# Kernel tuning notes

Measured on AMD Instinct MI355X. Metric: run time of the kernel, lower is better.

The kernel has to match this reference:

```python
import jax, jax.numpy as jnp
import numpy as np

N = 50000      # nodes
E = 1_600_000  # edges
F_IN = 128     # in_dim
H = 4          # heads
C = 32         # hidden_dim per head  (H*C == 128)
G = 64         # graphs in batch
HID2 = 64      # 2*hidden_dim
OUT = 10       # output_dim


def seg_softmax(logits, seg, num):
    # softmax over entries sharing the same segment id (leading axis)
    m = jax.ops.segment_max(logits, seg, num_segments=num)
    e = jnp.exp(logits - m[seg])
    s = jax.ops.segment_sum(e, seg, num_segments=num)
    return e / s[seg]


def gat_conv(x, src, dst, W, a_src, a_dst, b):
    # PyG GATConv (concat=True, negative_slope=0.2, self-loops added)
    h = (x @ W).reshape(N, H, C)                     # [N,H,C]
    loop = jnp.arange(N, dtype=src.dtype)
    s = jnp.concatenate([src, loop])                 # [E+N]
    d = jnp.concatenate([dst, loop])
    al_s = jnp.sum(h * a_src[None], axis=-1)         # [N,H]
    al_d = jnp.sum(h * a_dst[None], axis=-1)
    logits = jax.nn.leaky_relu(al_s[s] + al_d[d], 0.2)   # [E+N,H]
    alpha = seg_softmax(logits, d, N)                # softmax over incoming edges per dst
    msg = alpha[:, :, None] * h[s]                   # [E+N,H,C]
    out = jax.ops.segment_sum(msg, d, num_segments=N)    # [N,H,C]
    return out.reshape(N, H * C) + b


def setup_inputs() -> dict:
    key = jax.random.key(0)
    ks = jax.random.split(key, 16)
    x = jax.random.normal(ks[0], (N, F_IN), dtype=jnp.float32)
    src = jax.random.randint(ks[1], (E,), 0, N, dtype=jnp.int64)
    dst = jax.random.randint(ks[2], (E,), 0, N, dtype=jnp.int64)
    dst = jnp.where(src == dst, (dst + 1) % N, dst)  # GATConv removes self-loops then re-adds them
    edge_index = jnp.stack([src, dst])
    batch = jnp.sort(jax.random.randint(ks[3], (N,), 0, G, dtype=jnp.int64))
    g = lambda k, shp, fan: jax.random.normal(k, shp, dtype=jnp.float32) / np.sqrt(fan)
    return {
        "x": x, "edge_index": edge_index, "batch": batch,
        "W1": g(ks[4], (F_IN, H * C), F_IN), "a_src1": g(ks[5], (H, C), C), "a_dst1": g(ks[6], (H, C), C), "b1": jnp.zeros((H * C,), jnp.float32),
        "W2": g(ks[7], (H * C, H * C), H * C), "a_src2": g(ks[8], (H, C), C), "a_dst2": g(ks[9], (H, C), C), "b2": jnp.zeros((H * C,), jnp.float32),
        "gate_w": g(ks[10], (H * C, 1), H * C), "gate_b": jnp.zeros((1,), jnp.float32),
        "lin_w": g(ks[11], (H * C, HID2), H * C), "lin_b": jnp.zeros((HID2,), jnp.float32),
        "cls_w": g(ks[12], (HID2, OUT), HID2), "cls_b": jnp.zeros((OUT,), jnp.float32),
    }


def reference(x, edge_index, batch, W1, a_src1, a_dst1, b1, W2, a_src2, a_dst2, b2,
              gate_w, gate_b, lin_w, lin_b, cls_w, cls_b):
    src, dst = edge_index[0], edge_index[1]
    layers = [(W1, a_src1, a_dst1, b1), (W2, a_src2, a_dst2, b2)]
    hg = None
    h = x
    for (W, a_s, a_d, b) in layers:
        h = gat_conv(h, src, dst, W, a_s, a_d, b)
        h = jax.nn.relu(h)
        # per-graph softmax over nodes (dim=0 within each graph), per feature column
        h = seg_softmax(h, batch, G)
        # GlobalAttention pooling: gated segment-softmax sum
        gate = h @ gate_w + gate_b                    # [N,1]
        gate = seg_softmax(gate, batch, G)
        pooled = jax.ops.segment_sum(gate * h, batch, num_segments=G)  # [G, H*C]
        hg = pooled if hg is None else hg + pooled
    out = jax.nn.relu(hg @ lin_w + lin_b)             # dropout is identity in eval mode
    out = out @ cls_w + cls_b                         # [G, OUT]
    return out
```

## Files before the change

### kernel.cpp

```cpp
#include <hip/hip_runtime.h>
#include <hip/hip_fp16.h>
#include <math.h>

constexpr int N    = 50000;
constexpr int E    = 1600000;
constexpr int FD   = 128;
constexpr int H    = 4;
constexpr int G    = 64;
constexpr int NCH  = 16;
constexpr int OUT  = 10;

constexpr int NBIN   = (N + 255) / 256;
constexpr int EPB    = 4096;
constexpr int NBLK_E = (E + EPB - 1) / EPB;

#define DEV __device__ __forceinline__

DEV void fma4(float4& a, float s, const float4& w) {
    a.x = fmaf(s, w.x, a.x); a.y = fmaf(s, w.y, a.y);
    a.z = fmaf(s, w.z, a.z); a.w = fmaf(s, w.w, a.w);
}

DEV float lrelu_exp(float z) {
    return __expf(z > 0.f ? z : 0.2f * z);
}

union HF4 {
    float2  f;
    __half2 h[2];
};

DEV void fmah(float4& a, float w, const HF4& u) {
    float2 lo = __half22float2(u.h[0]);
    float2 hi = __half22float2(u.h[1]);
    a.x = fmaf(w, lo.x, a.x); a.y = fmaf(w, lo.y, a.y);
    a.z = fmaf(w, hi.x, a.z); a.w = fmaf(w, hi.y, a.w);
}

DEV float4 load4f(const float* p) { return *(const float4*)p; }
DEV float4 load4f(const __half* p) {
    HF4 u; u.f = *(const float2*)p;
    float2 lo = __half22float2(u.h[0]);
    float2 hi = __half22float2(u.h[1]);
    return make_float4(lo.x, lo.y, hi.x, hi.y);
}

__global__ void k_setup(const int* __restrict__ batch, int* __restrict__ gs,
                        int* __restrict__ hist, float* __restrict__ hg,
                        float* __restrict__ S1, float* __restrict__ S2,
                        float* __restrict__ Eg) {
    int i = blockIdx.x * 256 + threadIdx.x;
    if (i < NBIN) hist[i] = 0;
    if (i < 2 * G * FD) hg[i] = 0.f;
    if (i < G * FD) { S1[i] = 0.f; S2[i] = 0.f; }
    if (i < 2 * G) Eg[i] = 0.f;
    if (i < N) {
        int b  = batch[i];
        int pb = (i == 0) ? -1 : batch[i - 1];
        for (int g = pb + 1; g <= b; ++g) gs[g] = i;
        if (i == N - 1) for (int g = b + 1; g <= G; ++g) gs[g] = N;
    }
}

__global__ __launch_bounds__(256)
void k_hist(const int* __restrict__ dst, int* __restrict__ hist) {
    __shared__ int lh[NBIN];
    int t = threadIdx.x;
    for (int i = t; i < NBIN; i += 256) lh[i] = 0;
    __syncthreads();
    int base = blockIdx.x * EPB;
#pragma unroll
    for (int j = 0; j < EPB / 256; ++j) {
        int e = base + j * 256 + t;
        if (e < E) atomicAdd(&lh[dst[e] >> 8], 1);
    }
    __syncthreads();
    for (int i = t; i < NBIN; i += 256) if (lh[i]) atomicAdd(&hist[i], lh[i]);
}

__global__ __launch_bounds__(256)
void k_binscan(const int* __restrict__ hist, int* __restrict__ binbase,
               int* __restrict__ cursor, int* __restrict__ off) {
    __shared__ int sh[256];
    int t = threadIdx.x;
    int v = (t < NBIN) ? hist[t] : 0;
    sh[t] = v;
    __syncthreads();
    for (int d = 1; d < 256; d <<= 1) {
        int add = (t >= d) ? sh[t - d] : 0;
        __syncthreads();
        sh[t] += add;
        __syncthreads();
    }
    if (t < NBIN) {
        binbase[t] = sh[t] - v;
        cursor[t]  = sh[t] - v;
    }
    if (t == NBIN - 1) binbase[NBIN] = sh[t];
    if (t == 0) off[N] = E;
}

__global__ __launch_bounds__(256)
void k_partition(const int* __restrict__ src, const int* __restrict__ dst,
                 int* __restrict__ cursor, unsigned int* __restrict__ part) {
    __shared__ int lh[NBIN];
    __shared__ int gb[NBIN];
    int t = threadIdx.x;
    for (int i = t; i < NBIN; i += 256) lh[i] = 0;
    __syncthreads();
    int base = blockIdx.x * EPB;
    unsigned int pk[EPB / 256];
    int          pr[EPB / 256];
#pragma unroll
    for (int j = 0; j < EPB / 256; ++j) {
        int e = base + j * 256 + t;
        if (e < E) {
            int d = dst[e];
            int b = d >> 8;
            int r = atomicAdd(&lh[b], 1);
            pk[j] = (unsigned)src[e] | ((unsigned)(d & 255) << 16);
            pr[j] = (b << 16) | r;
        } else pr[j] = -1;
    }
    __syncthreads();
    for (int i = t; i < NBIN; i += 256) gb[i] = atomicAdd(&cursor[i], lh[i]);
    __syncthreads();
#pragma unroll
    for (int j = 0; j < EPB / 256; ++j) {
        if (pr[j] >= 0) {
            int b = pr[j] >> 16, r = pr[j] & 0xFFFF;
            part[gb[b] + r] = pk[j];
        }
    }
}

__global__ __launch_bounds__(256)
void k_fine(const unsigned int* __restrict__ part, const int* __restrict__ binbase,
            int* __restrict__ off, int* __restrict__ col) {
    __shared__ int lh[256], lo[256], lc[256];
    int b = blockIdx.x, t = threadIdx.x;
    int s = binbase[b], e = binbase[b + 1];
    lh[t] = 0; lc[t] = 0;
    __syncthreads();
    for (int i = s + t; i < e; i += 256) atomicAdd(&lh[part[i] >> 16], 1);
    __syncthreads();
    int v = lh[t];
    lo[t] = v;
    __syncthreads();
    for (int d = 1; d < 256; d <<= 1) {
        int add = (t >= d) ? lo[t - d] : 0;
        __syncthreads();
        lo[t] += add;
        __syncthreads();
    }
    int ex = lo[t] - v;
    __syncthreads();
    lo[t] = ex;
    __syncthreads();
    int node = b * 256 + t;
    if (node < N) off[node] = s + ex;
    for (int i = s + t; i < e; i += 256) {
        unsigned p = part[i];
        int dl = p >> 16;
        int r = atomicAdd(&lc[dl], 1);
        col[s + lo[dl] + r] = (int)(p & 0xFFFFu);
    }
}

template <typename TIn>
__global__ __launch_bounds__(256, 2)
void k_gemm_al(const TIn* __restrict__ X, const float* __restrict__ W,
               const float* __restrict__ a_s, const float* __restrict__ a_d,
               __half* __restrict__ hw, float* __restrict__ als, float* __restrict__ ald)
{
    __shared__ float xs[128][128];
    int r0 = blockIdx.x * 128;
    int t  = threadIdx.x;

    for (int i = 0; i < 16; ++i) {
        int f   = i * 256 + t;
        int row = f >> 5;
        int colf = (f & 31) * 4;
        float4 v = make_float4(0.f, 0.f, 0.f, 0.f);
        if (r0 + row < N) v = load4f(X + (size_t)(r0 + row) * FD + colf);
        *(float4*)(&xs[row][colf]) = v;
    }
    __syncthreads();

    int ct = t & 31;
    int rt = t >> 5;
    int c4 = ct * 4;
    int rb = rt * 16;

    float4 acc[16];
#pragma unroll
    for (int r = 0; r < 16; ++r) acc[r] = make_float4(0.f, 0.f, 0.f, 0.f);

    for (int k = 0; k < FD; k += 4) {
        float4 wv0 = *(const float4*)(W + (size_t)(k + 0) * FD + c4);
        float4 wv1 = *(const float4*)(W + (size_t)(k + 1) * FD + c4);
        float4 wv2 = *(const float4*)(W + (size_t)(k + 2) * FD + c4);
        float4 wv3 = *(const float4*)(W + (size_t)(k + 3) * FD + c4);
#pragma unroll
        for (int r = 0; r < 16; ++r) {
            float4 xv = *(const float4*)(&xs[rb + r][k]);
            fma4(acc[r], xv.x, wv0);
            fma4(acc[r], xv.y, wv1);
            fma4(acc[r], xv.z, wv2);
            fma4(acc[r], xv.w, wv3);
        }
    }

    int h  = c4 >> 5;
    int j0 = c4 & 31;
    float as0 = a_s[h * 32 + j0 + 0], as1 = a_s[h * 32 + j0 + 1];
    float as2 = a_s[h * 32 + j0 + 2], as3 = a_s[h * 32 + j0 + 3];
    float ad0 = a_d[h * 32 + j0 + 0], ad1 = a_d[h * 32 + j0 + 1];
    float ad2 = a_d[h * 32 + j0 + 2], ad3 = a_d[h * 32 + j0 + 3];

#pragma unroll
    for (int r = 0; r < 16; ++r) {
        int row = r0 + rb + r;
        bool valid = row < N;
        if (valid) {
            HF4 u;
            u.h[0] = __floats2half2_rn(acc[r].x, acc[r].y);
            u.h[1] = __floats2half2_rn(acc[r].z, acc[r].w);
            *(float2*)(hw + (size_t)row * FD + c4) = u.f;
        }
        float ps = acc[r].x * as0 + acc[r].y * as1 + acc[r].z * as2 + acc[r].w * as3;
        float pd = acc[r].x * ad0 + acc[r].y * ad1 + acc[r].z * ad2 + acc[r].w * ad3;
#pragma unroll
        for (int m = 1; m < 8; m <<= 1) {
            ps += __shfl_xor(ps, m, 64);
            pd += __shfl_xor(pd, m, 64);
        }
        if ((ct & 7) == 0 && valid) {
            als[row * H + h] = ps;
            ald[row * H + h] = pd;
        }
    }
}

__global__ __launch_bounds__(256)
void k_agg(const __half* __restrict__ hw, const float* __restrict__ als,
           const float* __restrict__ ald, const int* __restrict__ off,
           const int* __restrict__ col, const float* __restrict__ bias,
           __half* __restrict__ h1)
{
    int n = blockIdx.x * 4 + (threadIdx.x >> 6);
    if (n >= N) return;
    int l = threadIdx.x & 63;
    int q = l >> 5;
    int p = l & 31;
    int h = p >> 3;
    float adn = ald[n * H + h];

    float4 acc = make_float4(0.f, 0.f, 0.f, 0.f);
    float sumw;
    {
        float w = q ? 0.f : lrelu_exp(als[n * H + h] + adn);
        HF4 u; u.f = *(const float2*)(hw + (size_t)n * FD + 4 * p);
        fmah(acc, w, u);
        sumw = w;
    }

    int ib = off[n];
    int deg = off[n + 1] - ib;
    int j = 0;
    for (; j + 8 <= deg; j += 8) {
        int s0 = col[ib + j + 0 + q];
        int s1 = col[ib + j + 2 + q];
        int s2 = col[ib + j + 4 + q];
        int s3 = col[ib + j + 6 + q];
        float z0 = als[s0 * H + h];
        float z1 = als[s1 * H + h];
        float z2 = als[s2 * H + h];
        float z3 = als[s3 * H + h];
        HF4 u0; u0.f = *(const float2*)(hw + (size_t)s0 * FD + 4 * p);
        HF4 u1; u1.f = *(const float2*)(hw + (size_t)s1 * FD + 4 * p);
        HF4 u2; u2.f = *(const float2*)(hw + (size_t)s2 * FD + 4 * p);
        HF4 u3; u3.f = *(const float2*)(hw + (size_t)s3 * FD + 4 * p);
        float w0 = lrelu_exp(z0 + adn);
        float w1 = lrelu_exp(z1 + adn);
        float w2 = lrelu_exp(z2 + adn);
        float w3 = lrelu_exp(z3 + adn);
        fmah(acc, w0, u0);
        fmah(acc, w1, u1);
        fmah(acc, w2, u2);
        fmah(acc, w3, u3);
        sumw += w0 + w1 + w2 + w3;
    }
    for (; j + 2 <= deg; j += 2) {
        int s = col[ib + j + q];
        float w = lrelu_exp(als[s * H + h] + adn);
        HF4 u; u.f = *(const float2*)(hw + (size_t)s * FD + 4 * p);
        fmah(acc, w, u);
        sumw += w;
    }
    if (j < deg) {
        int s = q ? n : col[ib + j];
        float w = q ? 0.f : lrelu_exp(als[s * H + h] + adn);
        HF4 u; u.f = *(const float2*)(hw + (size_t)s * FD + 4 * p);
        fmah(acc, w, u);
        sumw += w;
    }

    acc.x += __shfl_xor(acc.x, 32, 64);
    acc.y += __shfl_xor(acc.y, 32, 64);
    acc.z += __shfl_xor(acc.z, 32, 64);
    acc.w += __shfl_xor(acc.w, 32, 64);
    sumw  += __shfl_xor(sumw,  32, 64);

    if (q == 0) {
        float inv = 1.f / sumw;
        float4 b4 = *(const float4*)(bias + 4 * p);
        float4 o;
        o.x = fmaf(acc.x, inv, b4.x);
        o.y = fmaf(acc.y, inv, b4.y);
        o.z = fmaf(acc.z, inv, b4.z);
        o.w = fmaf(acc.w, inv, b4.w);
        o.x = o.x > 0.f ? o.x : 0.f;
        o.y = o.y > 0.f ? o.y : 0.f;
        o.z = o.z > 0.f ? o.z : 0.f;
        o.w = o.w > 0.f ? o.w : 0.f;
        HF4 u;
        u.h[0] = __floats2half2_rn(o.x, o.y);
        u.h[1] = __floats2half2_rn(o.z, o.w);
        *(float2*)(h1 + (size_t)n * FD + 4 * p) = u.f;
    }
}

__global__ __launch_bounds__(256)
void k_colsum(const __half* __restrict__ h1, const int* __restrict__ gs,
              float* __restrict__ S)
{
    __shared__ float sh[256][4];
    int g = blockIdx.x, ch = blockIdx.y;
    int t = threadIdx.x;
    int p = t & 31, hf = t >> 5;
    int s = gs[g], e = gs[g + 1];
    int per = (e - s + NCH - 1) / NCH;
    int ns = s + ch * per;
    int ne = min(ns + per, e);
    if (ns >= ne) return;
    float4 acc = make_float4(0.f, 0.f, 0.f, 0.f);
    for (int n = ns + hf; n < ne; n += 8) {
        HF4 u; u.f = *(const float2*)(h1 + (size_t)n * FD + 4 * p);
        float2 lo = __half22float2(u.h[0]);
        float2 hi = __half22float2(u.h[1]);
        acc.x += __expf(lo.x); acc.y += __expf(lo.y);
        acc.z += __expf(hi.x); acc.w += __expf(hi.y);
    }
    sh[t][0] = acc.x; sh[t][1] = acc.y; sh[t][2] = acc.z; sh[t][3] = acc.w;
    __syncthreads();
    if (t < 32) {
        float4 a = make_float4(0.f, 0.f, 0.f, 0.f);
#pragma unroll
        for (int j = 0; j < 8; ++j) {
            a.x += sh[j * 32 + t][0]; a.y += sh[j * 32 + t][1];
            a.z += sh[j * 32 + t][2]; a.w += sh[j * 32 + t][3];
        }
        atomicAdd(&S[g * FD + 4 * t + 0], a.x);
        atomicAdd(&S[g * FD + 4 * t + 1], a.y);
        atomicAdd(&S[g * FD + 4 * t + 2], a.z);
        atomicAdd(&S[g * FD + 4 * t + 3], a.w);
    }
}

__global__ __launch_bounds__(256)
void k_softmax_gate(const __half* __restrict__ h1, const int* __restrict__ batch,
                    const float* __restrict__ S, const float* __restrict__ gw,
                    const float* __restrict__ gb, __half* __restrict__ hsm,
                    float* __restrict__ egl)
{
    int n = blockIdx.x * 8 + (threadIdx.x >> 5);
    if (n >= N) return;
    int p = threadIdx.x & 31;
    int g = batch[n];
    HF4 u; u.f = *(const float2*)(h1 + (size_t)n * FD + 4 * p);
    float2 lo = __half22float2(u.h[0]);
    float2 hi = __half22float2(u.h[1]);
    float4 sv = *(const float4*)(S + g * FD + 4 * p);
    float vx = __expf(lo.x) / sv.x;
    float vy = __expf(lo.y) / sv.y;
    float vz = __expf(hi.x) / sv.z;
    float vw = __expf(hi.y) / sv.w;
    HF4 o;
    o.h[0] = __floats2half2_rn(vx, vy);
    o.h[1] = __floats2half2_rn(vz, vw);
    *(float2*)(hsm + (size_t)n * FD + 4 * p) = o.f;
    float4 gv = *(const float4*)(gw + 4 * p);
    float pl = vx * gv.x + vy * gv.y + vz * gv.z + vw * gv.w;
#pragma unroll
    for (int m = 1; m < 32; m <<= 1) pl += __shfl_xor(pl, m, 32);
    if (p == 0) egl[n] = __expf(pl + gb[0]);
}

__global__ __launch_bounds__(256)
void k_pool(const __half* __restrict__ hsm, const float* __restrict__ egl,
            const int* __restrict__ gs, float* __restrict__ hgl,
            float* __restrict__ Egl)
{
    __shared__ float sh[256][4];
    __shared__ float se[8];
    int g = blockIdx.x, ch = blockIdx.y;
    int t = threadIdx.x;
    int p = t & 31, hf = t >> 5;
    int s = gs[g], e = gs[g + 1];
    int per = (e - s + NCH - 1) / NCH;
    int ns = s + ch * per;
    int ne = min(ns + per, e);
    if (ns >= ne) return;
    float4 acc = make_float4(0.f, 0.f, 0.f, 0.f);
    float esum = 0.f;
    for (int n = ns + hf; n < ne; n += 8) {
        float eg = egl[n];
        if (p == 0) esum += eg;
        HF4 u; u.f = *(const float2*)(hsm + (size_t)n * FD + 4 * p);
        float2 lo = __half22float2(u.h[0]);
        float2 hi = __half22float2(u.h[1]);
        acc.x = fmaf(eg, lo.x, acc.x); acc.y = fmaf(eg, lo.y, acc.y);
        acc.z = fmaf(eg, hi.x, acc.z); acc.w = fmaf(eg, hi.y, acc.w);
    }
    sh[t][0] = acc.x; sh[t][1] = acc.y; sh[t][2] = acc.z; sh[t][3] = acc.w;
    if (p == 0) se[hf] = esum;
    __syncthreads();
    if (t < 32) {
        float4 a = make_float4(0.f, 0.f, 0.f, 0.f);
#pragma unroll
        for (int j = 0; j < 8; ++j) {
            a.x += sh[j * 32 + t][0]; a.y += sh[j * 32 + t][1];
            a.z += sh[j * 32 + t][2]; a.w += sh[j * 32 + t][3];
        }
        atomicAdd(&hgl[g * FD + 4 * t + 0], a.x);
        atomicAdd(&hgl[g * FD + 4 * t + 1], a.y);
        atomicAdd(&hgl[g * FD + 4 * t + 2], a.z);
        atomicAdd(&hgl[g * FD + 4 * t + 3], a.w);
    } else if (t == 32) {
        float es = 0.f;
#pragma unroll
        for (int j = 0; j < 8; ++j) es += se[j];
        atomicAdd(&Egl[g], es);
    }
}

__global__ __launch_bounds__(64)
void k_head(const float* __restrict__ hg, const float* __restrict__ Eg,
            const float* __restrict__ lin_w, const float* __restrict__ lin_b,
            const float* __restrict__ cls_w, const float* __restrict__ cls_b,
            float* __restrict__ out)
{
    __shared__ float hrow[128];
    __shared__ float tbuf[64];
    int g = blockIdx.x, j = threadIdx.x;
    float e1 = Eg[g], e2 = Eg[G + g];
    float i1 = e1 > 0.f ? 1.f / e1 : 0.f;
    float i2 = e2 > 0.f ? 1.f / e2 : 0.f;
    const float* hg1 = hg;
    const float* hg2 = hg + G * FD;
    hrow[j]      = hg1[g * FD + j] * i1      + hg2[g * FD + j] * i2;
    hrow[j + 64] = hg1[g * FD + j + 64] * i1 + hg2[g * FD + j + 64] * i2;
    __syncthreads();
    float a = lin_b[j];
    for (int c = 0; c < 128; ++c) a = fmaf(hrow[c], lin_w[c * 64 + j], a);
    tbuf[j] = a > 0.f ? a : 0.f;
    __syncthreads();
    if (j < OUT) {
        float o = cls_b[j];
        for (int k = 0; k < 64; ++k) o = fmaf(tbuf[k], cls_w[k * OUT + j], o);
        out[g * OUT + j] = o;
    }
}

extern "C" void kernel_launch(void* const* d_in, const int* in_sizes, int n_in,
                              void* d_out, int out_size, void* d_ws, size_t ws_size,
                              hipStream_t stream)
{
    const float* x      = (const float*)d_in[0];
    const int*   ei     = (const int*)d_in[1];
    const int*   src    = ei;
    const int*   dst    = ei + E;
    const int*   batch  = (const int*)d_in[2];
    const float* W1     = (const float*)d_in[3];
    const float* as1    = (const float*)d_in[4];
    const float* ad1    = (const float*)d_in[5];
    const float* b1     = (const float*)d_in[6];
    const float* W2     = (const float*)d_in[7];
    const float* as2    = (const float*)d_in[8];
    const float* ad2    = (const float*)d_in[9];
    const float* b2     = (const float*)d_in[10];
    const float* gate_w = (const float*)d_in[11];
    const float* gate_b = (const float*)d_in[12];
    const float* lin_w  = (const float*)d_in[13];
    const float* lin_b  = (const float*)d_in[14];
    const float* cls_w  = (const float*)d_in[15];
    const float* cls_b  = (const float*)d_in[16];
    float* outp = (float*)d_out;

    char* ws = (char*)d_ws;
    size_t o = 0;
    auto alloc = [&](size_t bytes) -> char* {
        char* p = ws + o;
        o = (o + bytes + 255) & ~(size_t)255;
        return p;
    };

    int*    gs      = (int*)alloc((G + 1) * sizeof(int));
    int*    hist    = (int*)alloc(256 * sizeof(int));
    int*    binbase = (int*)alloc(256 * sizeof(int));
    int*    cursor  = (int*)alloc(256 * sizeof(int));
    int*    off     = (int*)alloc((N + 1) * sizeof(int));
    int*    col     = (int*)alloc((size_t)E * sizeof(int));
    float*  als     = (float*)alloc((size_t)N * H * sizeof(float));
    float*  ald     = (float*)alloc((size_t)N * H * sizeof(float));
    __half* hw      = (__half*)alloc((size_t)N * FD * sizeof(__half));
    __half* h1      = (__half*)alloc((size_t)N * FD * sizeof(__half));
    __half* hsm     = (__half*)alloc((size_t)N * FD * sizeof(__half));
    float*  S1      = (float*)alloc((size_t)G * FD * sizeof(float));
    float*  S2      = (float*)alloc((size_t)G * FD * sizeof(float));
    float*  Eg      = (float*)alloc((size_t)2 * G * sizeof(float));
    float*  egl     = (float*)alloc((size_t)N * sizeof(float));
    float*  hg      = (float*)alloc((size_t)2 * G * FD * sizeof(float));

    unsigned int* part = (unsigned int*)hw;

    int nbN = (N + 255) / 256;

    k_setup<<<nbN, 256, 0, stream>>>(batch, gs, hist, hg, S1, S2, Eg);
    k_hist<<<NBLK_E, 256, 0, stream>>>(dst, hist);
    k_binscan<<<1, 256, 0, stream>>>(hist, binbase, cursor, off);
    k_partition<<<NBLK_E, 256, 0, stream>>>(src, dst, cursor, part);
    k_fine<<<NBIN, 256, 0, stream>>>(part, binbase, off, col);

    auto run_layer = [&](auto hin, const float* W, const float* a_s,
                         const float* a_d, const float* bias, float* S,
                         float* hgl, float* Egl) {
        k_gemm_al<<<(N + 127) / 128, 256, 0, stream>>>(hin, W, a_s, a_d, hw, als, ald);
        k_agg<<<(N + 3) / 4, 256, 0, stream>>>(hw, als, ald, off, col, bias, h1);
        k_colsum<<<dim3(G, NCH), 256, 0, stream>>>(h1, gs, S);
        k_softmax_gate<<<(N + 7) / 8, 256, 0, stream>>>(h1, batch, S, gate_w, gate_b, hsm, egl);
        k_pool<<<dim3(G, NCH), 256, 0, stream>>>(hsm, egl, gs, hgl, Egl);
    };

    run_layer(x, W1, as1, ad1, b1, S1, hg, Eg);
    run_layer((const __half*)hsm, W2, as2, ad2, b2, S2, hg + G * FD, Eg + G);

    k_head<<<G, 64, 0, stream>>>(hg, Eg, lin_w, lin_b, cls_w, cls_b, outp);
}
```

Before: 402.0 us.

## Use fp16 MFMA for node GEMM and fold attention vectors into weights

Replaces the fp32 FMA GEMM with an fp16 MFMA 16x16x32 kernel that stages X and a pre-transposed fp16 W in padded LDS. The attention logits are computed as X·(W·a) using per-layer precomputed WSD vectors, so they no longer need a reduction over GEMM outputs. A small prep kernel builds the fp16 transposed weights and folded vectors. Costs: the layer-1 input x is now rounded to fp16, and the output stores are scalar half writes that may coalesce poorly.

```diff
diff --git a/kernel.cpp b/kernel.cpp
--- a/kernel.cpp
+++ b/kernel.cpp
@@ -14,12 +14,12 @@
 constexpr int EPB    = 4096;
 constexpr int NBLK_E = (E + EPB - 1) / EPB;
 
+constexpr int LDH = 136;
+
 #define DEV __device__ __forceinline__
 
-DEV void fma4(float4& a, float s, const float4& w) {
-    a.x = fmaf(s, w.x, a.x); a.y = fmaf(s, w.y, a.y);
-    a.z = fmaf(s, w.z, a.z); a.w = fmaf(s, w.w, a.w);
-}
+typedef _Float16 h8 __attribute__((ext_vector_type(8)));
+typedef float f32x4 __attribute__((ext_vector_type(4)));
 
 DEV float lrelu_exp(float z) {
     return __expf(z > 0.f ? z : 0.2f * z);
@@ -35,14 +35,6 @@
     float2 hi = __half22float2(u.h[1]);
     a.x = fmaf(w, lo.x, a.x); a.y = fmaf(w, lo.y, a.y);
     a.z = fmaf(w, hi.x, a.z); a.w = fmaf(w, hi.y, a.w);
-}
-
-DEV float4 load4f(const float* p) { return *(const float4*)p; }
-DEV float4 load4f(const __half* p) {
-    HF4 u; u.f = *(const float2*)p;
-    float2 lo = __half22float2(u.h[0]);
-    float2 hi = __half22float2(u.h[1]);
-    return make_float4(lo.x, lo.y, hi.x, hi.y);
 }
 
 __global__ void k_setup(const int* __restrict__ batch, int* __restrict__ gs,
@@ -63,6 +55,31 @@
 }
 
 __global__ __launch_bounds__(256)
+void k_wprep(const float* __restrict__ W, const float* __restrict__ a_s,
+             const float* __restrict__ a_d, _Float16* __restrict__ Wt,
+             float* __restrict__ WSD)
+{
+    int t = threadIdx.x;
+    for (int pass = 0; pass < 64; ++pass) {
+        int idx = pass * 256 + t;
+        int k = idx >> 7, c = idx & 127;
+        Wt[c * FD + k] = (_Float16)W[idx];
+    }
+    if (t < FD) {
+        for (int h = 0; h < H; ++h) {
+            float ss = 0.f, sd = 0.f;
+            for (int j = 0; j < 32; ++j) {
+                float wv = W[t * FD + h * 32 + j];
+                ss = fmaf(wv, a_s[h * 32 + j], ss);
+                sd = fmaf(wv, a_d[h * 32 + j], sd);
+            }
+            WSD[t * 8 + h * 2]     = ss;
+            WSD[t * 8 + h * 2 + 1] = sd;
+        }
+    }
+}
+
+__global__ __launch_bounds__(256)
 void k_hist(const int* __restrict__ dst, int* __restrict__ hist) {
     __shared__ int lh[NBIN];
     int t = threadIdx.x;
@@ -169,75 +186,105 @@
 
 template <typename TIn>
 __global__ __launch_bounds__(256, 2)
-void k_gemm_al(const TIn* __restrict__ X, const float* __restrict__ W,
-               const float* __restrict__ a_s, const float* __restrict__ a_d,
-               __half* __restrict__ hw, float* __restrict__ als, float* __restrict__ ald)
-{
-    __shared__ float xs[128][128];
+void k_gemm_mfma(const TIn* __restrict__ X, const _Float16* __restrict__ Wt,
+                 const float* __restrict__ WSD, __half* __restrict__ hw,
+                 float* __restrict__ als, float* __restrict__ ald)
+{
+    __shared__ _Float16 Xh[128 * LDH];
+    __shared__ _Float16 Wl[128 * LDH];
+    __shared__ float    wsd[128 * 8];
     int r0 = blockIdx.x * 128;
     int t  = threadIdx.x;
 
-    for (int i = 0; i < 16; ++i) {
-        int f   = i * 256 + t;
-        int row = f >> 5;
-        int colf = (f & 31) * 4;
-        float4 v = make_float4(0.f, 0.f, 0.f, 0.f);
-        if (r0 + row < N) v = load4f(X + (size_t)(r0 + row) * FD + colf);
-        *(float4*)(&xs[row][colf]) = v;
-    }
-    __syncthreads();
-
-    int ct = t & 31;
-    int rt = t >> 5;
-    int c4 = ct * 4;
-    int rb = rt * 16;
-
-    float4 acc[16];
-#pragma unroll
-    for (int r = 0; r < 16; ++r) acc[r] = make_float4(0.f, 0.f, 0.f, 0.f);
-
-    for (int k = 0; k < FD; k += 4) {
-        float4 wv0 = *(const float4*)(W + (size_t)(k + 0) * FD + c4);
-        float4 wv1 = *(const float4*)(W + (size_t)(k + 1) * FD + c4);
-        float4 wv2 = *(const float4*)(W + (size_t)(k + 2) * FD + c4);
-        float4 wv3 = *(const float4*)(W + (size_t)(k + 3) * FD + c4);
-#pragma unroll
-        for (int r = 0; r < 16; ++r) {
-            float4 xv = *(const float4*)(&xs[rb + r][k]);
-            fma4(acc[r], xv.x, wv0);
-            fma4(acc[r], xv.y, wv1);
-            fma4(acc[r], xv.z, wv2);
-            fma4(acc[r], xv.w, wv3);
-        }
-    }
-
-    int h  = c4 >> 5;
-    int j0 = c4 & 31;
-    float as0 = a_s[h * 32 + j0 + 0], as1 = a_s[h * 32 + j0 + 1];
-    float as2 = a_s[h * 32 + j0 + 2], as3 = a_s[h * 32 + j0 + 3];
-    float ad0 = a_d[h * 32 + j0 + 0], ad1 = a_d[h * 32 + j0 + 1];
-    float ad2 = a_d[h * 32 + j0 + 2], ad3 = a_d[h * 32 + j0 + 3];
-
-#pragma unroll
-    for (int r = 0; r < 16; ++r) {
-        int row = r0 + rb + r;
-        bool valid = row < N;
-        if (valid) {
-            HF4 u;
-            u.h[0] = __floats2half2_rn(acc[r].x, acc[r].y);
-            u.h[1] = __floats2half2_rn(acc[r].z, acc[r].w);
-            *(float2*)(hw + (size_t)row * FD + c4) = u.f;
-        }
-        float ps = acc[r].x * as0 + acc[r].y * as1 + acc[r].z * as2 + acc[r].w * as3;
-        float pd = acc[r].x * ad0 + acc[r].y * ad1 + acc[r].z * ad2 + acc[r].w * ad3;
-#pragma unroll
-        for (int m = 1; m < 8; m <<= 1) {
-            ps += __shfl_xor(ps, m, 64);
-            pd += __shfl_xor(pd, m, 64);
-        }
-        if ((ct & 7) == 0 && valid) {
-            als[row * H + h] = ps;
-            ald[row * H + h] = pd;
+#pragma unroll
+    for (int pass = 0; pass < 8; ++pass) {
+        int idx  = pass * 2048 + t * 8;
+        int row  = idx >> 7;
+        int colh = idx & 127;
+        h8 v = {};
+        if (r0 + row < N) {
+            if constexpr (sizeof(TIn) == 4) {
+                const float4* sp = (const float4*)(X + (size_t)(r0 + row) * FD + colh);
+                float4 f0 = sp[0], f1 = sp[1];
+                v[0] = (_Float16)f0.x; v[1] = (_Float16)f0.y;
+                v[2] = (_Float16)f0.z; v[3] = (_Float16)f0.w;
+                v[4] = (_Float16)f1.x; v[5] = (_Float16)f1.y;
+                v[6] = (_Float16)f1.z; v[7] = (_Float16)f1.w;
+            } else {
+                v = *(const h8*)((const _Float16*)X + (size_t)(r0 + row) * FD + colh);
+            }
+        }
+        *(h8*)&Xh[row * LDH + colh] = v;
+        *(h8*)&Wl[row * LDH + colh] = *(const h8*)(Wt + idx);
+    }
+    if (t < 128) {
+        *(float4*)&wsd[t * 8]     = *(const float4*)(WSD + t * 8);
+        *(float4*)&wsd[t * 8 + 4] = *(const float4*)(WSD + t * 8 + 4);
+    }
+    __syncthreads();
+
+    {
+        int row = t >> 1, p = t & 1;
+        float s0 = 0.f, s1 = 0.f, s2 = 0.f, s3 = 0.f;
+        for (int j = 0; j < FD; j += 8) {
+            h8 xv = *(h8*)&Xh[row * LDH + j];
+#pragma unroll
+            for (int u = 0; u < 8; ++u) {
+                float xf = (float)xv[u];
+                float4 wq = *(float4*)&wsd[(j + u) * 8 + p * 4];
+                s0 = fmaf(xf, wq.x, s0); s1 = fmaf(xf, wq.y, s1);
+                s2 = fmaf(xf, wq.z, s2); s3 = fmaf(xf, wq.w, s3);
+            }
+        }
+        int grow = r0 + row;
+        if (grow < N) {
+            als[grow * H + 2 * p + 0] = s0;
+            ald[grow * H + 2 * p + 0] = s1;
+            als[grow * H + 2 * p + 1] = s2;
+            ald[grow * H + 2 * p + 1] = s3;
+        }
+    }
+
+    int w = t >> 6, l = t & 63;
+    int lr = l & 15, kg = l >> 4;
+    int koff = kg * 8;
+
+    h8 a[2][4];
+#pragma unroll
+    for (int rt = 0; rt < 2; ++rt)
+#pragma unroll
+        for (int kk = 0; kk < 4; ++kk)
+            a[rt][kk] = *(h8*)&Xh[(w * 32 + rt * 16 + lr) * LDH + kk * 32 + koff];
+
+    f32x4 acc[2][8] = {};
+#pragma unroll
+    for (int ct = 0; ct < 8; ++ct) {
+        h8 b0 = *(h8*)&Wl[(ct * 16 + lr) * LDH + 0 * 32 + koff];
+        h8 b1 = *(h8*)&Wl[(ct * 16 + lr) * LDH + 1 * 32 + koff];
+        h8 b2 = *(h8*)&Wl[(ct * 16 + lr) * LDH + 2 * 32 + koff];
+        h8 b3 = *(h8*)&Wl[(ct * 16 + lr) * LDH + 3 * 32 + koff];
+#pragma unroll
+        for (int rt = 0; rt < 2; ++rt) {
+            f32x4 c = acc[rt][ct];
+            c = __builtin_amdgcn_mfma_f32_16x16x32_f16(a[rt][0], b0, c, 0, 0, 0);
+            c = __builtin_amdgcn_mfma_f32_16x16x32_f16(a[rt][1], b1, c, 0, 0, 0);
+            c = __builtin_amdgcn_mfma_f32_16x16x32_f16(a[rt][2], b2, c, 0, 0, 0);
+            c = __builtin_amdgcn_mfma_f32_16x16x32_f16(a[rt][3], b3, c, 0, 0, 0);
+            acc[rt][ct] = c;
+        }
+    }
+
+#pragma unroll
+    for (int rt = 0; rt < 2; ++rt) {
+        int rbase = r0 + w * 32 + rt * 16 + kg * 4;
+#pragma unroll
+        for (int reg = 0; reg < 4; ++reg) {
+            int grow = rbase + reg;
+            if (grow < N) {
+#pragma unroll
+                for (int ct = 0; ct < 8; ++ct)
+                    hw[(size_t)grow * FD + ct * 16 + lr] = __float2half(acc[rt][ct][reg]);
+            }
         }
     }
 }
@@ -506,45 +553,50 @@
         return p;
     };
 
-    int*    gs      = (int*)alloc((G + 1) * sizeof(int));
-    int*    hist    = (int*)alloc(256 * sizeof(int));
-    int*    binbase = (int*)alloc(256 * sizeof(int));
-    int*    cursor  = (int*)alloc(256 * sizeof(int));
-    int*    off     = (int*)alloc((N + 1) * sizeof(int));
-    int*    col     = (int*)alloc((size_t)E * sizeof(int));
-    float*  als     = (float*)alloc((size_t)N * H * sizeof(float));
-    float*  ald     = (float*)alloc((size_t)N * H * sizeof(float));
-    __half* hw      = (__half*)alloc((size_t)N * FD * sizeof(__half));
-    __half* h1      = (__half*)alloc((size_t)N * FD * sizeof(__half));
-    __half* hsm     = (__half*)alloc((size_t)N * FD * sizeof(__half));
-    float*  S1      = (float*)alloc((size_t)G * FD * sizeof(float));
-    float*  S2      = (float*)alloc((size_t)G * FD * sizeof(float));
-    float*  Eg      = (float*)alloc((size_t)2 * G * sizeof(float));
-    float*  egl     = (float*)alloc((size_t)N * sizeof(float));
-    float*  hg      = (float*)alloc((size_t)2 * G * FD * sizeof(float));
+    int*      gs      = (int*)alloc((G + 1) * sizeof(int));
+    int*      hist    = (int*)alloc(256 * sizeof(int));
+    int*      binbase = (int*)alloc(256 * sizeof(int));
+    int*      cursor  = (int*)alloc(256 * sizeof(int));
+    int*      off     = (int*)alloc((N + 1) * sizeof(int));
+    int*      col     = (int*)alloc((size_t)E * sizeof(int));
+    float*    als     = (float*)alloc((size_t)N * H * sizeof(float));
+    float*    ald     = (float*)alloc((size_t)N * H * sizeof(float));
+    __half*   hw      = (__half*)alloc((size_t)N * FD * sizeof(__half));
+    __half*   h1      = (__half*)alloc((size_t)N * FD * sizeof(__half));
+    __half*   hsm     = (__half*)alloc((size_t)N * FD * sizeof(__half));
+    float*    S1      = (float*)alloc((size_t)G * FD * sizeof(float));
+    float*    S2      = (float*)alloc((size_t)G * FD * sizeof(float));
+    float*    Eg      = (float*)alloc((size_t)2 * G * sizeof(float));
+    float*    egl     = (float*)alloc((size_t)N * sizeof(float));
+    float*    hg      = (float*)alloc((size_t)2 * G * FD * sizeof(float));
+    _Float16* Wt1     = (_Float16*)alloc((size_t)FD * FD * sizeof(_Float16));
+    _Float16* Wt2     = (_Float16*)alloc((size_t)FD * FD * sizeof(_Float16));
+    float*    WSD1    = (float*)alloc((size_t)FD * 8 * sizeof(float));
+    float*    WSD2    = (float*)alloc((size_t)FD * 8 * sizeof(float));
 
     unsigned int* part = (unsigned int*)hw;
 
     int nbN = (N + 255) / 256;
 
+    k_wprep<<<1, 256, 0, stream>>>(W1, as1, ad1, Wt1, WSD1);
+    k_wprep<<<1, 256, 0, stream>>>(W2, as2, ad2, Wt2, WSD2);
     k_setup<<<nbN, 256, 0, stream>>>(batch, gs, hist, hg, S1, S2, Eg);
     k_hist<<<NBLK_E, 256, 0, stream>>>(dst, hist);
     k_binscan<<<1, 256, 0, stream>>>(hist, binbase, cursor, off);
     k_partition<<<NBLK_E, 256, 0, stream>>>(src, dst, cursor, part);
     k_fine<<<NBIN, 256, 0, stream>>>(part, binbase, off, col);
 
-    auto run_layer = [&](auto hin, const float* W, const float* a_s,
-                         const float* a_d, const float* bias, float* S,
-                         float* hgl, float* Egl) {
-        k_gemm_al<<<(N + 127) / 128, 256, 0, stream>>>(hin, W, a_s, a_d, hw, als, ald);
+    auto run_layer = [&](auto hin, const _Float16* Wt, const float* WSD,
+                         const float* bias, float* S, float* hgl, float* Egl) {
+        k_gemm_mfma<<<(N + 127) / 128, 256, 0, stream>>>(hin, Wt, WSD, hw, als, ald);
         k_agg<<<(N + 3) / 4, 256, 0, stream>>>(hw, als, ald, off, col, bias, h1);
         k_colsum<<<dim3(G, NCH), 256, 0, stream>>>(h1, gs, S);
         k_softmax_gate<<<(N + 7) / 8, 256, 0, stream>>>(h1, batch, S, gate_w, gate_b, hsm, egl);
         k_pool<<<dim3(G, NCH), 256, 0, stream>>>(hsm, egl, gs, hgl, Egl);
     };
 
-    run_layer(x, W1, as1, ad1, b1, S1, hg, Eg);
-    run_layer((const __half*)hsm, W2, as2, ad2, b2, S2, hg + G * FD, Eg + G);
+    run_layer(x, Wt1, WSD1, b1, S1, hg, Eg);
+    run_layer((const __half*)hsm, Wt2, WSD2, b2, S2, hg + G * FD, Eg + G);
 
     k_head<<<G, 64, 0, stream>>>(hg, Eg, lin_w, lin_b, cls_w, cls_b, outp);
 }
```

Measured after the change: 401.0 us. No clear change (-0.2%).
